# Kernel tuning notes

Hardware: AMD Instinct MI355X
Metric: run time of the kernel (lower is better)

## Reference

```python
import jax, jax.numpy as jnp
import numpy as np

B_, L_, D_, N_ = 4, 4096, 64, 16
DT = 0.1
EPS = 1e-6


def _complex_log(x):
    # log|x| (clamped) + i*pi for negative entries, matching torch impl
    real = jnp.log(jnp.maximum(jnp.abs(x), EPS))
    imag = jnp.where(x < 0, jnp.float32(np.pi), jnp.float32(0.0))
    return jax.lax.complex(real, imag)


def _clogaddexp(a, b):
    # stable complex log(exp(a)+exp(b)) using max of real parts
    m = jnp.maximum(a.real, b.real)
    return jnp.log(jnp.exp(a - m) + jnp.exp(b - m)) + m


def _clogcumsumexp(x, axis):
    return jax.lax.associative_scan(_clogaddexp, x, axis=axis)


def setup_inputs() -> dict:
    key = jax.random.key(0)
    ks = jax.random.split(key, 6)
    x = jax.random.normal(ks[0], (B_, L_, D_), jnp.float32)
    s = 1.0 / np.sqrt(D_)
    Wb = jax.random.uniform(ks[1], (N_, D_), jnp.float32, -s, s)
    bb = jax.random.uniform(ks[2], (N_,), jnp.float32, -s, s)
    Wc = jax.random.uniform(ks[3], (N_, D_), jnp.float32, -s, s)
    bc = jax.random.uniform(ks[4], (N_,), jnp.float32, -s, s)
    Wd = jax.random.uniform(ks[5], (1, D_), jnp.float32, -s, s)
    bd = jnp.zeros((1,), jnp.float32)
    # S4D-Real init: A_n = -(n+1), repeated over input_dim rows -> (D, N)
    A = jnp.tile(-(jnp.arange(N_, dtype=jnp.float32) + 1.0)[None, :], (D_, 1))
    return {"x": x, "A": A, "Wb": Wb, "bb": bb, "Wc": Wc, "bc": bc,
            "Wd": Wd, "bd": bd}


def reference(x, A, Wb, bb, Wc, bc, Wd, bd):
    # projections: (b,l,n)
    Bm = x @ Wb.T + bb
    Cm = x @ Wc.T + bc
    # delta network: softplus(linear(x)) + dt, broadcast to input_dim
    delta = jax.nn.softplus(x @ Wd.T + bd) + DT            # (b,l,1)
    dt = jnp.broadcast_to(delta, x.shape)                  # (b,l,d)
    # discretize
    tmp = A * dt[..., None]                                # (b,l,d,n)
    A_bar = jnp.exp(tmp)
    delta_B = jnp.einsum('bld,bln->bldn', dt, Bm)
    B_bar = (A_bar - 1.0) * delta_B / (tmp + EPS)
    term2 = B_bar * x[..., None]                           # (b,l,d,n)
    # parallel scan via complex log-cumsum-exp trick
    log_a = _complex_log(A_bar)
    log_b = _complex_log(term2)
    a_star = jnp.cumsum(log_a, axis=1)                     # (b,l,d,n) complex
    t = _clogcumsumexp(log_b - a_star, axis=1)
    scan = jnp.exp(a_star + t).real                        # (b,l,d,n)
    return jnp.sum(scan * Cm[:, :, None, :], axis=-1)      # (b,l,d)
```

## Files before the change

kernel.cpp:

```cpp
#include <hip/hip_runtime.h>

#define B_ 4
#define L_ 4096
#define D_ 64
#define N_ 16
#define CHUNK 16
#define NCHUNK (L_ / CHUNK)
#define TOTCHUNK (B_ * NCHUNK)
#define PROW 48

constexpr float DT_  = 0.1f;
constexpr float EPS_ = 1e-6f;

__global__ __launch_bounds__(64) void proj_kernel(
    const float* __restrict__ x,  const float* __restrict__ A,
    const float* __restrict__ Wb, const float* __restrict__ bb,
    const float* __restrict__ Wc, const float* __restrict__ bc,
    const float* __restrict__ Wd, const float* __restrict__ bd,
    float* __restrict__ P, float* __restrict__ Wcor, float* __restrict__ Cdec)
{
    const int gc    = blockIdx.x;
    const int batch = gc >> 8;
    const int c     = gc & (NCHUNK - 1);
    const int lane  = threadIdx.x;
    const int base0 = batch * L_ + c * CHUNK;

    __shared__ float xs[CHUNK * D_];
    __shared__ float pbuf[CHUNK * PROW];
    __shared__ float wbuf[CHUNK * N_];

    const float4* xg  = (const float4*)(x + (size_t)base0 * D_);
    float4*       xsv = (float4*)xs;
    #pragma unroll
    for (int i = 0; i < 4; i++) xsv[i * 64 + lane] = xg[i * 64 + lane];

    const int n  = lane & 15;
    const int qt = lane >> 4;
    float wB[16], wC[16];
    {
        const float4* wb4 = (const float4*)(Wb + n * D_ + qt * 16);
        const float4* wc4 = (const float4*)(Wc + n * D_ + qt * 16);
        #pragma unroll
        for (int j = 0; j < 4; j++) {
            float4 b4 = wb4[j], c4 = wc4[j];
            wB[4*j+0] = b4.x; wB[4*j+1] = b4.y; wB[4*j+2] = b4.z; wB[4*j+3] = b4.w;
            wC[4*j+0] = c4.x; wC[4*j+1] = c4.y; wC[4*j+2] = c4.z; wC[4*j+3] = c4.w;
        }
    }
    const float wd  = Wd[lane];
    const float bd0 = bd[0];
    const float An  = A[n];
    const float bB  = bb[n];
    const float bC  = bc[n];

    __syncthreads();

    float r[CHUNK];
    #pragma unroll
    for (int p = 0; p < CHUNK; p++) r[p] = xs[p * D_ + lane] * wd;
    #pragma unroll
    for (int m = 32; m >= 1; m >>= 1) {
        #pragma unroll
        for (int p = 0; p < CHUNK; p++) r[p] += __shfl_xor(r[p], m, 64);
    }
    float delta[CHUNK];
    #pragma unroll
    for (int p = 0; p < CHUNK; p++) {
        float z = r[p] + bd0;
        delta[p] = fmaxf(z, 0.0f) + log1pf(expf(-fabsf(z))) + DT_;
    }

    float av[CHUNK], cv[CHUNK];
    #pragma unroll
    for (int p = 0; p < CHUNK; p++) {
        const float4* xs4 = (const float4*)(xs + p * D_ + qt * 16);
        float accB = 0.0f, accC = 0.0f;
        #pragma unroll
        for (int j = 0; j < 4; j++) {
            float4 v = xs4[j];
            accB += v.x * wB[4*j+0] + v.y * wB[4*j+1] + v.z * wB[4*j+2] + v.w * wB[4*j+3];
            accC += v.x * wC[4*j+0] + v.y * wC[4*j+1] + v.z * wC[4*j+2] + v.w * wC[4*j+3];
        }
        accB += __shfl_xor(accB, 16, 64);  accB += __shfl_xor(accB, 32, 64);
        accC += __shfl_xor(accC, 16, 64);  accC += __shfl_xor(accC, 32, 64);

        float Bm  = accB + bB;
        float Cmv = accC + bC;
        float tmp = An * delta[p];
        float a   = expf(tmp);
        float g   = (a - 1.0f) * delta[p] * Bm / (tmp + EPS_);
        av[p] = a;  cv[p] = Cmv;
        if      (qt == 0) pbuf[p * PROW + n]      = a;
        else if (qt == 1) pbuf[p * PROW + 16 + n] = g;
        else if (qt == 2) pbuf[p * PROW + 32 + n] = Cmv;
    }

    float cum = 1.0f;
    #pragma unroll
    for (int p = 0; p < CHUNK; p++) {
        cum *= av[p];
        if (qt == 3) wbuf[p * N_ + n] = cv[p] * cum;
    }
    if (qt == 3) Cdec[gc * N_ + n] = cum;
    __syncthreads();

    {
        float4*       Pg  = (float4*)(P + (size_t)gc * (CHUNK * PROW));
        const float4* pb4 = (const float4*)pbuf;
        Pg[lane]       = pb4[lane];
        Pg[64 + lane]  = pb4[64 + lane];
        Pg[128 + lane] = pb4[128 + lane];
        ((float4*)(Wcor + (size_t)gc * (CHUNK * N_)))[lane] = ((const float4*)wbuf)[lane];
    }
}

__global__ __launch_bounds__(64) void scan_kernel(
    const float* __restrict__ x, const float* __restrict__ P,
    float* __restrict__ S, float* __restrict__ out)
{
    const int gc    = blockIdx.x;
    const int batch = gc >> 8;
    const int c     = gc & (NCHUNK - 1);
    const int lane  = threadIdx.x;
    const int base0 = batch * L_ + c * CHUNK;

    float xq[CHUNK];
    #pragma unroll
    for (int p = 0; p < CHUNK; p++)
        xq[p] = x[(size_t)(base0 + p) * D_ + lane];

    const float* pp = P + (size_t)gc * (CHUNK * PROW);

    float h[N_];
    #pragma unroll
    for (int i = 0; i < N_; i++) h[i] = 0.0f;

    #pragma unroll
    for (int p = 0; p < CHUNK; p++) {
        const float4* row = (const float4*)(pp + p * PROW);
        float acc = 0.0f;
        #pragma unroll
        for (int q = 0; q < 4; q++) {
            float4 a4 = row[q];
            float4 g4 = row[4 + q];
            float4 c4 = row[8 + q];
            h[4*q+0] = a4.x * h[4*q+0] + g4.x * xq[p];  acc += c4.x * h[4*q+0];
            h[4*q+1] = a4.y * h[4*q+1] + g4.y * xq[p];  acc += c4.y * h[4*q+1];
            h[4*q+2] = a4.z * h[4*q+2] + g4.z * xq[p];  acc += c4.z * h[4*q+2];
            h[4*q+3] = a4.w * h[4*q+3] + g4.w * xq[p];  acc += c4.w * h[4*q+3];
        }
        out[(size_t)(base0 + p) * D_ + lane] = acc;
    }
    #pragma unroll
    for (int i = 0; i < N_; i++)
        S[(size_t)(gc * N_ + i) * D_ + lane] = h[i];
}

#define G_ 32
__global__ __launch_bounds__(64) void combine(
    float* __restrict__ S, const float* __restrict__ Cdec)
{
    const int b = blockIdx.x >> 4;
    const int n = blockIdx.x & 15;
    const int d = threadIdx.x;
    const int cb = b * NCHUNK;

    float*       baseS = S    + (size_t)(cb * N_ + n) * D_ + d;
    const float* baseA = Cdec + cb * N_ + n;

    float run = 0.0f;
    float sbuf[G_], abuf[G_];
    #pragma unroll
    for (int j = 0; j < G_; j++) {
        sbuf[j] = baseS[(size_t)j * (N_ * D_)];
        abuf[j] = baseA[j * N_];
    }
    for (int cc = 0; cc < NCHUNK; cc += G_) {
        const int cn = (cc + G_ < NCHUNK) ? (cc + G_) : cc;
        float t[G_], u[G_];
        #pragma unroll
        for (int j = 0; j < G_; j++) {
            t[j] = baseS[(size_t)(cn + j) * (N_ * D_)];
            u[j] = baseA[(cn + j) * N_];
        }
        #pragma unroll
        for (int j = 0; j < G_; j++) {
            baseS[(size_t)(cc + j) * (N_ * D_)] = run;
            run = abuf[j] * run + sbuf[j];
        }
        #pragma unroll
        for (int j = 0; j < G_; j++) { sbuf[j] = t[j]; abuf[j] = u[j]; }
    }
}

__global__ __launch_bounds__(64) void apply_kernel(
    const float* __restrict__ Wcor, const float* __restrict__ S,
    float* __restrict__ out)
{
    const int gc    = blockIdx.x;
    const int batch = gc >> 8;
    const int c     = gc & (NCHUNK - 1);
    const int lane  = threadIdx.x;
    const int base0 = batch * L_ + c * CHUNK;

    float hi[N_];
    #pragma unroll
    for (int i = 0; i < N_; i++)
        hi[i] = S[(size_t)(gc * N_ + i) * D_ + lane];

    const float* wrow = Wcor + (size_t)gc * (CHUNK * N_);
    #pragma unroll
    for (int p = 0; p < CHUNK; p++) {
        const float4* w4 = (const float4*)(wrow + p * N_);
        float acc = 0.0f;
        #pragma unroll
        for (int q = 0; q < 4; q++) {
            float4 w = w4[q];
            acc += w.x * hi[4*q+0] + w.y * hi[4*q+1]
                 + w.z * hi[4*q+2] + w.w * hi[4*q+3];
        }
        const size_t idx = (size_t)(base0 + p) * D_ + lane;
        out[idx] = out[idx] + acc;
    }
}

extern "C" void kernel_launch(void* const* d_in, const int* in_sizes, int n_in,
                              void* d_out, int out_size, void* d_ws, size_t ws_size,
                              hipStream_t stream)
{
    const float* x  = (const float*)d_in[0];
    const float* A  = (const float*)d_in[1];
    const float* Wb = (const float*)d_in[2];
    const float* bb = (const float*)d_in[3];
    const float* Wc = (const float*)d_in[4];
    const float* bc = (const float*)d_in[5];
    const float* Wd = (const float*)d_in[6];
    const float* bd = (const float*)d_in[7];
    float* out = (float*)d_out;

    float* P    = (float*)d_ws;
    float* Wcor = P    + (size_t)TOTCHUNK * CHUNK * PROW;
    float* S    = Wcor + (size_t)TOTCHUNK * CHUNK * N_;
    float* Cdec = S    + (size_t)TOTCHUNK * N_ * D_;

    proj_kernel<<<TOTCHUNK, 64, 0, stream>>>(x, A, Wb, bb, Wc, bc, Wd, bd,
                                             P, Wcor, Cdec);
    scan_kernel<<<TOTCHUNK, 64, 0, stream>>>(x, P, S, out);
    combine<<<B_ * N_, 64, 0, stream>>>(S, Cdec);
    apply_kernel<<<TOTCHUNK, 64, 0, stream>>>(Wcor, S, out);
}
```

Baseline: 117.2 us.

## Fuse projection and intra-chunk scan into one kernel via shared memory

Merges proj_kernel and scan_kernel so the per-chunk a/g/C coefficients stay in LDS instead of going out to a global P buffer and being reloaded. This removes one launch and a global round trip. The delta projection is now computed as a partial dot product alongside B and C, replacing a six-step shuffle reduction per row. apply_kernel stages Wcor through shared memory. The scan loop is no longer explicitly unrolled.

```diff
diff --git a/kernel.cpp b/kernel.cpp
--- a/kernel.cpp
+++ b/kernel.cpp
@@ -7,17 +7,17 @@
 #define CHUNK 16
 #define NCHUNK (L_ / CHUNK)
 #define TOTCHUNK (B_ * NCHUNK)
-#define PROW 48
 
 constexpr float DT_  = 0.1f;
 constexpr float EPS_ = 1e-6f;
 
-__global__ __launch_bounds__(64) void proj_kernel(
+__global__ __launch_bounds__(64) void proj_scan_kernel(
     const float* __restrict__ x,  const float* __restrict__ A,
     const float* __restrict__ Wb, const float* __restrict__ bb,
     const float* __restrict__ Wc, const float* __restrict__ bc,
     const float* __restrict__ Wd, const float* __restrict__ bd,
-    float* __restrict__ P, float* __restrict__ Wcor, float* __restrict__ Cdec)
+    float* __restrict__ S, float* __restrict__ Cdec,
+    float* __restrict__ Wcor, float* __restrict__ out)
 {
     const int gc    = blockIdx.x;
     const int batch = gc >> 8;
@@ -26,7 +26,8 @@
     const int base0 = batch * L_ + c * CHUNK;
 
     __shared__ float xs[CHUNK * D_];
-    __shared__ float pbuf[CHUNK * PROW];
+    __shared__ float ag[CHUNK * 32];
+    __shared__ float cm[CHUNK * N_];
     __shared__ float wbuf[CHUNK * N_];
 
     const float4* xg  = (const float4*)(x + (size_t)base0 * D_);
@@ -36,18 +37,19 @@
 
     const int n  = lane & 15;
     const int qt = lane >> 4;
-    float wB[16], wC[16];
+    float wB[16], wC[16], wD[16];
     {
         const float4* wb4 = (const float4*)(Wb + n * D_ + qt * 16);
         const float4* wc4 = (const float4*)(Wc + n * D_ + qt * 16);
+        const float4* wd4 = (const float4*)(Wd + qt * 16);
         #pragma unroll
         for (int j = 0; j < 4; j++) {
-            float4 b4 = wb4[j], c4 = wc4[j];
+            float4 b4 = wb4[j], c4 = wc4[j], d4 = wd4[j];
             wB[4*j+0] = b4.x; wB[4*j+1] = b4.y; wB[4*j+2] = b4.z; wB[4*j+3] = b4.w;
             wC[4*j+0] = c4.x; wC[4*j+1] = c4.y; wC[4*j+2] = c4.z; wC[4*j+3] = c4.w;
-        }
-    }
-    const float wd  = Wd[lane];
+            wD[4*j+0] = d4.x; wD[4*j+1] = d4.y; wD[4*j+2] = d4.z; wD[4*j+3] = d4.w;
+        }
+    }
     const float bd0 = bd[0];
     const float An  = A[n];
     const float bB  = bb[n];
@@ -55,68 +57,113 @@
 
     __syncthreads();
 
-    float r[CHUNK];
-    #pragma unroll
-    for (int p = 0; p < CHUNK; p++) r[p] = xs[p * D_ + lane] * wd;
-    #pragma unroll
-    for (int m = 32; m >= 1; m >>= 1) {
-        #pragma unroll
-        for (int p = 0; p < CHUNK; p++) r[p] += __shfl_xor(r[p], m, 64);
-    }
-    float delta[CHUNK];
-    #pragma unroll
-    for (int p = 0; p < CHUNK; p++) {
-        float z = r[p] + bd0;
-        delta[p] = fmaxf(z, 0.0f) + log1pf(expf(-fabsf(z))) + DT_;
-    }
-
     float av[CHUNK], cv[CHUNK];
     #pragma unroll
     for (int p = 0; p < CHUNK; p++) {
         const float4* xs4 = (const float4*)(xs + p * D_ + qt * 16);
-        float accB = 0.0f, accC = 0.0f;
+        float accB = 0.0f, accC = 0.0f, accD = 0.0f;
         #pragma unroll
         for (int j = 0; j < 4; j++) {
             float4 v = xs4[j];
             accB += v.x * wB[4*j+0] + v.y * wB[4*j+1] + v.z * wB[4*j+2] + v.w * wB[4*j+3];
             accC += v.x * wC[4*j+0] + v.y * wC[4*j+1] + v.z * wC[4*j+2] + v.w * wC[4*j+3];
+            accD += v.x * wD[4*j+0] + v.y * wD[4*j+1] + v.z * wD[4*j+2] + v.w * wD[4*j+3];
         }
         accB += __shfl_xor(accB, 16, 64);  accB += __shfl_xor(accB, 32, 64);
         accC += __shfl_xor(accC, 16, 64);  accC += __shfl_xor(accC, 32, 64);
-
-        float Bm  = accB + bB;
-        float Cmv = accC + bC;
-        float tmp = An * delta[p];
-        float a   = expf(tmp);
-        float g   = (a - 1.0f) * delta[p] * Bm / (tmp + EPS_);
+        accD += __shfl_xor(accD, 16, 64);  accD += __shfl_xor(accD, 32, 64);
+
+        float z     = accD + bd0;
+        float delta = fmaxf(z, 0.0f) + log1pf(expf(-fabsf(z))) + DT_;
+        float Bm    = accB + bB;
+        float Cmv   = accC + bC;
+        float tmp   = An * delta;
+        float a     = expf(tmp);
+        float g     = (a - 1.0f) * delta * Bm / (tmp + EPS_);
         av[p] = a;  cv[p] = Cmv;
-        if      (qt == 0) pbuf[p * PROW + n]      = a;
-        else if (qt == 1) pbuf[p * PROW + 16 + n] = g;
-        else if (qt == 2) pbuf[p * PROW + 32 + n] = Cmv;
-    }
-
-    float cum = 1.0f;
-    #pragma unroll
-    for (int p = 0; p < CHUNK; p++) {
-        cum *= av[p];
-        if (qt == 3) wbuf[p * N_ + n] = cv[p] * cum;
-    }
-    if (qt == 3) Cdec[gc * N_ + n] = cum;
+        if      (qt == 0) ag[p * 32 + n]      = a;
+        else if (qt == 1) ag[p * 32 + 16 + n] = g;
+        else if (qt == 2) cm[p * 16 + n]      = Cmv;
+    }
+
+    {
+        float cum = 1.0f;
+        #pragma unroll
+        for (int p = 0; p < CHUNK; p++) {
+            cum *= av[p];
+            if (qt == 3) wbuf[p * N_ + n] = cv[p] * cum;
+        }
+        if (qt == 3) Cdec[gc * N_ + n] = cum;
+    }
     __syncthreads();
 
-    {
-        float4*       Pg  = (float4*)(P + (size_t)gc * (CHUNK * PROW));
-        const float4* pb4 = (const float4*)pbuf;
-        Pg[lane]       = pb4[lane];
-        Pg[64 + lane]  = pb4[64 + lane];
-        Pg[128 + lane] = pb4[128 + lane];
-        ((float4*)(Wcor + (size_t)gc * (CHUNK * N_)))[lane] = ((const float4*)wbuf)[lane];
-    }
-}
-
-__global__ __launch_bounds__(64) void scan_kernel(
-    const float* __restrict__ x, const float* __restrict__ P,
-    float* __restrict__ S, float* __restrict__ out)
+    ((float4*)(Wcor + (size_t)gc * (CHUNK * N_)))[lane] = ((const float4*)wbuf)[lane];
+
+    float h[N_];
+    #pragma unroll
+    for (int i = 0; i < N_; i++) h[i] = 0.0f;
+    for (int s = 0; s < CHUNK; s++) {
+        float xd = xs[s * D_ + lane];
+        const float4* row = (const float4*)(ag + s * 32);
+        const float4* crw = (const float4*)(cm + s * 16);
+        float acc = 0.0f;
+        #pragma unroll
+        for (int q = 0; q < 4; q++) {
+            float4 a4 = row[q];
+            float4 g4 = row[4 + q];
+            float4 c4 = crw[q];
+            h[4*q+0] = a4.x * h[4*q+0] + g4.x * xd;  acc += c4.x * h[4*q+0];
+            h[4*q+1] = a4.y * h[4*q+1] + g4.y * xd;  acc += c4.y * h[4*q+1];
+            h[4*q+2] = a4.z * h[4*q+2] + g4.z * xd;  acc += c4.z * h[4*q+2];
+            h[4*q+3] = a4.w * h[4*q+3] + g4.w * xd;  acc += c4.w * h[4*q+3];
+        }
+        out[(size_t)(base0 + s) * D_ + lane] = acc;
+    }
+    #pragma unroll
+    for (int i = 0; i < N_; i++)
+        S[(size_t)(gc * N_ + i) * D_ + lane] = h[i];
+}
+
+#define G_ 32
+__global__ __launch_bounds__(64) void combine(
+    float* __restrict__ S, const float* __restrict__ Cdec)
+{
+    const int b = blockIdx.x >> 4;
+    const int n = blockIdx.x & 15;
+    const int d = threadIdx.x;
+    const int cb = b * NCHUNK;
+
+    float*       baseS = S    + (size_t)(cb * N_ + n) * D_ + d;
+    const float* baseA = Cdec + cb * N_ + n;
+
+    float run = 0.0f;
+    float sbuf[G_], abuf[G_];
+    #pragma unroll
+    for (int j = 0; j < G_; j++) {
+        sbuf[j] = baseS[(size_t)j * (N_ * D_)];
+        abuf[j] = baseA[j * N_];
+    }
+    for (int cc = 0; cc < NCHUNK; cc += G_) {
+        const int cn = (cc + G_ < NCHUNK) ? (cc + G_) : cc;
+        float t[G_], u[G_];
+        #pragma unroll
+        for (int j = 0; j < G_; j++) {
+            t[j] = baseS[(size_t)(cn + j) * (N_ * D_)];
+            u[j] = baseA[(cn + j) * N_];
+        }
+        #pragma unroll
+        for (int j = 0; j < G_; j++) {
+            baseS[(size_t)(cc + j) * (N_ * D_)] = run;
+            run = abuf[j] * run + sbuf[j];
+        }
+        #pragma unroll
+        for (int j = 0; j < G_; j++) { sbuf[j] = t[j]; abuf[j] = u[j]; }
+    }
+}
+
+__global__ __launch_bounds__(64) void apply_kernel(
+    const float* __restrict__ Wcor, const float* __restrict__ S,
+    float* __restrict__ out)
 {
     const int gc    = blockIdx.x;
     const int batch = gc >> 8;
@@ -124,100 +171,26 @@
     const int lane  = threadIdx.x;
     const int base0 = batch * L_ + c * CHUNK;
 
-    float xq[CHUNK];
-    #pragma unroll
-    for (int p = 0; p < CHUNK; p++)
-        xq[p] = x[(size_t)(base0 + p) * D_ + lane];
-
-    const float* pp = P + (size_t)gc * (CHUNK * PROW);
-
-    float h[N_];
-    #pragma unroll
-    for (int i = 0; i < N_; i++) h[i] = 0.0f;
-
-    #pragma unroll
-    for (int p = 0; p < CHUNK; p++) {
-        const float4* row = (const float4*)(pp + p * PROW);
-        float acc = 0.0f;
-        #pragma unroll
-        for (int q = 0; q < 4; q++) {
-            float4 a4 = row[q];
-            float4 g4 = row[4 + q];
-            float4 c4 = row[8 + q];
-            h[4*q+0] = a4.x * h[4*q+0] + g4.x * xq[p];  acc += c4.x * h[4*q+0];
-            h[4*q+1] = a4.y * h[4*q+1] + g4.y * xq[p];  acc += c4.y * h[4*q+1];
-            h[4*q+2] = a4.z * h[4*q+2] + g4.z * xq[p];  acc += c4.z * h[4*q+2];
-            h[4*q+3] = a4.w * h[4*q+3] + g4.w * xq[p];  acc += c4.w * h[4*q+3];
-        }
-        out[(size_t)(base0 + p) * D_ + lane] = acc;
-    }
-    #pragma unroll
-    for (int i = 0; i < N_; i++)
-        S[(size_t)(gc * N_ + i) * D_ + lane] = h[i];
-}
-
-#define G_ 32
-__global__ __launch_bounds__(64) void combine(
-    float* __restrict__ S, const float* __restrict__ Cdec)
-{
-    const int b = blockIdx.x >> 4;
-    const int n = blockIdx.x & 15;
-    const int d = threadIdx.x;
-    const int cb = b * NCHUNK;
-
-    float*       baseS = S    + (size_t)(cb * N_ + n) * D_ + d;
-    const float* baseA = Cdec + cb * N_ + n;
-
-    float run = 0.0f;
-    float sbuf[G_], abuf[G_];
-    #pragma unroll
-    for (int j = 0; j < G_; j++) {
-        sbuf[j] = baseS[(size_t)j * (N_ * D_)];
-        abuf[j] = baseA[j * N_];
-    }
-    for (int cc = 0; cc < NCHUNK; cc += G_) {
-        const int cn = (cc + G_ < NCHUNK) ? (cc + G_) : cc;
-        float t[G_], u[G_];
-        #pragma unroll
-        for (int j = 0; j < G_; j++) {
-            t[j] = baseS[(size_t)(cn + j) * (N_ * D_)];
-            u[j] = baseA[(cn + j) * N_];
-        }
-        #pragma unroll
-        for (int j = 0; j < G_; j++) {
-            baseS[(size_t)(cc + j) * (N_ * D_)] = run;
-            run = abuf[j] * run + sbuf[j];
-        }
-        #pragma unroll
-        for (int j = 0; j < G_; j++) { sbuf[j] = t[j]; abuf[j] = u[j]; }
-    }
-}
-
-__global__ __launch_bounds__(64) void apply_kernel(
-    const float* __restrict__ Wcor, const float* __restrict__ S,
-    float* __restrict__ out)
-{
-    const int gc    = blockIdx.x;
-    const int batch = gc >> 8;
-    const int c     = gc & (NCHUNK - 1);
-    const int lane  = threadIdx.x;
-    const int base0 = batch * L_ + c * CHUNK;
+    __shared__ float wl[CHUNK * N_];
+
+    ((float4*)wl)[lane] = ((const float4*)(Wcor + (size_t)gc * (CHUNK * N_)))[lane];
 
     float hi[N_];
     #pragma unroll
     for (int i = 0; i < N_; i++)
         hi[i] = S[(size_t)(gc * N_ + i) * D_ + lane];
 
-    const float* wrow = Wcor + (size_t)gc * (CHUNK * N_);
+    __syncthreads();
+
     #pragma unroll
     for (int p = 0; p < CHUNK; p++) {
-        const float4* w4 = (const float4*)(wrow + p * N_);
+        const float4* crw = (const float4*)(wl + p * N_);
         float acc = 0.0f;
         #pragma unroll
         for (int q = 0; q < 4; q++) {
-            float4 w = w4[q];
-            acc += w.x * hi[4*q+0] + w.y * hi[4*q+1]
-                 + w.z * hi[4*q+2] + w.w * hi[4*q+3];
+            float4 w4 = crw[q];
+            acc += w4.x * hi[4*q+0] + w4.y * hi[4*q+1]
+                 + w4.z * hi[4*q+2] + w4.w * hi[4*q+3];
         }
         const size_t idx = (size_t)(base0 + p) * D_ + lane;
         out[idx] = out[idx] + acc;
@@ -238,14 +211,12 @@
     const float* bd = (const float*)d_in[7];
     float* out = (float*)d_out;
 
-    float* P    = (float*)d_ws;
-    float* Wcor = P    + (size_t)TOTCHUNK * CHUNK * PROW;
-    float* S    = Wcor + (size_t)TOTCHUNK * CHUNK * N_;
+    float* S    = (float*)d_ws;
     float* Cdec = S    + (size_t)TOTCHUNK * N_ * D_;
-
-    proj_kernel<<<TOTCHUNK, 64, 0, stream>>>(x, A, Wb, bb, Wc, bc, Wd, bd,
-                                             P, Wcor, Cdec);
-    scan_kernel<<<TOTCHUNK, 64, 0, stream>>>(x, P, S, out);
+    float* Wcor = Cdec + (size_t)TOTCHUNK * N_;
+
+    proj_scan_kernel<<<TOTCHUNK, 64, 0, stream>>>(x, A, Wb, bb, Wc, bc, Wd, bd,
+                                                  S, Cdec, Wcor, out);
     combine<<<B_ * N_, 64, 0, stream>>>(S, Cdec);
     apply_kernel<<<TOTCHUNK, 64, 0, stream>>>(Wcor, S, out);
 }
```

New measurement: 105.3 us. -10.2%, faster.
